# Kernel optimization log

Measured on AMD Instinct MI355X. Metric: run time of the kernel, lower is better.

The kernel has to match this reference:

```python
import jax, jax.numpy as jnp
import numpy as np
import math

EPS = 1e-5
HEADS = 8

def _lin(x, w, b):
    return x @ w.T + b

def _ln(x, g, b):
    m = x.mean(-1, keepdims=True)
    v = ((x - m) ** 2).mean(-1, keepdims=True)
    return (x - m) / jnp.sqrt(v + EPS) * g + b

def _bn_eval(x, g, b):
    # BatchNorm1d eval with init running stats (mean=0, var=1)
    return x / jnp.sqrt(1.0 + EPS) * g[None, :, None] + b[None, :, None]

def _conv1d(x, w, b, pad):
    y = jax.lax.conv_general_dilated(x, w, (1,), [(pad, pad)],
                                     dimension_numbers=('NCH', 'OIH', 'NCH'))
    return y + b[None, :, None]

def _interp_linear(x, out_len):
    # F.interpolate(mode='linear', align_corners=False) on last axis
    L = x.shape[-1]
    src = (jnp.arange(out_len) + 0.5) * (L / out_len) - 0.5
    src = jnp.clip(src, 0.0, L - 1)
    i0 = jnp.floor(src).astype(jnp.int32)
    i1 = jnp.minimum(i0 + 1, L - 1)
    w = (src - i0).astype(x.dtype)
    return x[..., i0] * (1.0 - w) + x[..., i1] * w

def setup_inputs():
    key = jax.random.key(0)
    ks = iter(jax.random.split(key, 64))
    def nrm(shape, scale=0.02):
        return jax.random.normal(next(ks), shape, dtype=jnp.float32) * scale
    B, T, N, H, HOR, C = 2, 64, 2048, 128, 24, 32
    return dict(
        x=jax.random.normal(next(ks), (B, T, N), dtype=jnp.float32),
        tc_w=nrm((C, 1, 3), 0.2), tc_b=jnp.zeros((C,)), tc_bn_g=jnp.ones((C,)), tc_bn_b=jnp.zeros((C,)),
        fp_w=nrm((H, C * T)), fp_b=jnp.zeros((H,)), fp_ln_g=jnp.ones((H,)), fp_ln_b=jnp.zeros((H,)),
        q_w=nrm((H, H)), q_b=jnp.zeros((H,)),
        k_w=nrm((H, H)), k_b=jnp.zeros((H,)),
        v_w=nrm((H, H)), v_b=jnp.zeros((H,)),
        o_w=nrm((H, H)), o_b=jnp.zeros((H,)),
        adj=nrm((1, HEADS, N, N), 0.02),
        s0_w=nrm((H, H, 1), 0.05), s0_b=jnp.zeros((H,)), s0_bn_g=jnp.ones((H,)), s0_bn_b=jnp.zeros((H,)),
        s1_w=nrm((H, H, 2), 0.05), s1_b=jnp.zeros((H,)), s1_bn_g=jnp.ones((H,)), s1_bn_b=jnp.zeros((H,)),
        fusion_weight=jnp.ones((2,)),
        fu_w=nrm((H, H)), fu_b=jnp.zeros((H,)), fu_ln_g=jnp.ones((H,)), fu_ln_b=jnp.zeros((H,)),
        pr1_w=nrm((H, H)), pr1_b=jnp.zeros((H,)), pr_ln_g=jnp.ones((H,)), pr_ln_b=jnp.zeros((H,)),
        pr2_w=nrm((HOR, H)), pr2_b=jnp.zeros((HOR,)),
        rg_w=nrm((HOR, H)), rg_b=jnp.zeros((HOR,)),
    )

def _forward(x, tc_w, tc_b, tc_bn_g, tc_bn_b, fp_w, fp_b, fp_ln_g, fp_ln_b,
             q_w, q_b, k_w, k_b, v_w, v_b, o_w, o_b, adj,
             s0_w, s0_b, s0_bn_g, s0_bn_b, s1_w, s1_b, s1_bn_g, s1_bn_b,
             fusion_weight, fu_w, fu_b, fu_ln_g, fu_ln_b,
             pr1_w, pr1_b, pr_ln_g, pr_ln_b, pr2_w, pr2_b, rg_w, rg_b):
    B, T, N = x.shape
    H = q_w.shape[0]
    hd = H // HEADS
    x_last = x[:, -1, :]                                  # (B, N)
    # temporal conv over the window per node
    xt = x.transpose(0, 2, 1).reshape(B * N, 1, T)
    f = jax.nn.relu(_bn_eval(_conv1d(xt, tc_w, tc_b, 1), tc_bn_g, tc_bn_b))
    f = f.reshape(B, N, -1)                               # (B, N, 32*T)
    feats = jax.nn.relu(_ln(_lin(f, fp_w, fp_b), fp_ln_g, fp_ln_b))
    # adaptive graph attention with learnable adjacency bias
    q = _lin(feats, q_w, q_b).reshape(B, N, HEADS, hd)
    k = _lin(feats, k_w, k_b).reshape(B, N, HEADS, hd)
    v = _lin(feats, v_w, v_b).reshape(B, N, HEADS, hd)
    scores = jnp.einsum('bnhd,bmhd->bhnm', q, k) / math.sqrt(hd) + adj
    attn = jax.nn.softmax(scores, axis=-1)                # (B, HEADS, N, N)
    reg = jnp.float32(1e-4) * jnp.mean(jnp.abs(attn))
    go = jnp.einsum('bhnm,bmhd->bnhd', attn, v).reshape(B, N, H)
    gf = _lin(go, o_w, o_b)                               # (B, N, H)
    # multi-scale fusion (conv over node axis, kernels 1 and 2)
    xc = gf.transpose(0, 2, 1)                            # (B, H, N)
    f0 = jax.nn.relu(_bn_eval(_conv1d(xc, s0_w, s0_b, 0), s0_bn_g, s0_bn_b))
    f1 = jax.nn.relu(_bn_eval(_conv1d(xc, s1_w, s1_b, 1), s1_bn_g, s1_bn_b))  # (B,H,N+1)
    f1 = _interp_linear(f1, N)
    alpha = jax.nn.softmax(fusion_weight)
    fused = (alpha[0] * f0 + alpha[1] * f1).transpose(0, 2, 1)
    ff = jax.nn.relu(_ln(_lin(fused, fu_w, fu_b), fu_ln_g, fu_ln_b))
    # progressive prediction refinement
    h = jax.nn.relu(_ln(_lin(ff, pr1_w, pr1_b), pr_ln_g, pr_ln_b))
    preds = _lin(h, pr2_w, pr2_b)                         # (B, N, horizon)
    gates = jax.nn.sigmoid(_lin(ff, rg_w, rg_b))
    refined = gates * x_last[..., None] + (1.0 - gates) * preds
    return refined.transpose(0, 2, 1), reg                # (B, horizon, N), scalar

def reference(x, tc_w, tc_b, tc_bn_g, tc_bn_b, fp_w, fp_b, fp_ln_g, fp_ln_b,
              q_w, q_b, k_w, k_b, v_w, v_b, o_w, o_b, adj,
              s0_w, s0_b, s0_bn_g, s0_bn_b, s1_w, s1_b, s1_bn_g, s1_bn_b,
              fusion_weight, fu_w, fu_b, fu_ln_g, fu_ln_b,
              pr1_w, pr1_b, pr_ln_g, pr_ln_b, pr2_w, pr2_b, rg_w, rg_b):
    return _forward(x, tc_w, tc_b, tc_bn_g, tc_bn_b, fp_w, fp_b, fp_ln_g, fp_ln_b,
                    q_w, q_b, k_w, k_b, v_w, v_b, o_w, o_b, adj,
                    s0_w, s0_b, s0_bn_g, s0_bn_b, s1_w, s1_b, s1_bn_g, s1_bn_b,
                    fusion_weight, fu_w, fu_b, fu_ln_g, fu_ln_b,
                    pr1_w, pr1_b, pr_ln_g, pr_ln_b, pr2_w, pr2_b, rg_w, rg_b)
```

## Files before the change

kernel.cpp:

```cpp
#include <hip/hip_runtime.h>

using f32x4  = __attribute__((ext_vector_type(4))) float;
using bf16x8 = __attribute__((ext_vector_type(8))) short;

#define DEV static __device__ __forceinline__

DEV unsigned short f2bf(float f){
  unsigned u = __float_as_uint(f);
  unsigned r = (u + 0x7FFFu + ((u >> 16) & 1u)) >> 16;
  return (unsigned short)r;
}

__global__ __launch_bounds__(256) void prep_conv_kernel(
    const float* __restrict__ fp_w, const float* __restrict__ q_w,
    const float* __restrict__ k_w, const float* __restrict__ v_w,
    const float* __restrict__ o_w, const float* __restrict__ s0_w,
    const float* __restrict__ s1_w, const float* __restrict__ fu_w,
    const float* __restrict__ pr1_w, const float* __restrict__ pr2_w,
    const float* __restrict__ rg_w,
    unsigned short* __restrict__ fpw_bf, unsigned short* __restrict__ wcat_bf,
    float* __restrict__ o_wT, float* __restrict__ fu_wT, float* __restrict__ pr1_wT,
    float* __restrict__ s0_wT, float* __restrict__ s1_wT0, float* __restrict__ s1_wT1,
    float* __restrict__ pr2_wT, float* __restrict__ rg_wT,
    const float* __restrict__ x, const float* __restrict__ tc_w,
    const float* __restrict__ tc_b, const float* __restrict__ bn_g,
    const float* __restrict__ bn_b, unsigned short* __restrict__ f){
  if (blockIdx.x < 512){
    int i = blockIdx.x * 256 + threadIdx.x;
    const int stride = 512 * 256;
    for (int idx = i; idx < 128 * 2048; idx += stride) fpw_bf[idx] = f2bf(fp_w[idx]);
    for (int idx = i; idx < 384 * 128; idx += stride){
      int c = idx >> 7, k = idx & 127;
      float v;
      if (c < 128)      v = q_w[c * 128 + k] * 0.25f;
      else if (c < 256) v = k_w[(c - 128) * 128 + k];
      else              v = v_w[(c - 256) * 128 + k];
      wcat_bf[idx] = f2bf(v);
    }
    for (int idx = i; idx < 128 * 128; idx += stride){
      int k = idx >> 7, c = idx & 127;
      o_wT[idx]   = o_w[c * 128 + k];
      fu_wT[idx]  = fu_w[c * 128 + k];
      pr1_wT[idx] = pr1_w[c * 128 + k];
      s0_wT[idx]  = s0_w[c * 128 + k];
      s1_wT0[idx] = s1_w[(c * 128 + k) * 2 + 0];
      s1_wT1[idx] = s1_w[(c * 128 + k) * 2 + 1];
    }
    for (int idx = i; idx < 128 * 24; idx += stride){
      int k = idx / 24, c = idx % 24;
      pr2_wT[idx] = pr2_w[c * 128 + k];
      rg_wT[idx]  = rg_w[c * 128 + k];
    }
  } else {
    int lane = threadIdx.x & 63;
    int w = threadIdx.x >> 6;
    int row = (blockIdx.x - 512) * 4 + w;
    int b = row >> 11, n = row & 2047;
    float xv = x[(size_t)(b * 64 + lane) * 2048 + n];
    float xm = __shfl_up(xv, 1, 64);   if (lane == 0)  xm = 0.f;
    float xp = __shfl_down(xv, 1, 64); if (lane == 63) xp = 0.f;
    const float inv = rsqrtf(1.0f + 1e-5f);
    unsigned short* frow = f + (size_t)row * 2048;
    #pragma unroll
    for (int c = 0; c < 32; c++){
      float y = xm * tc_w[c * 3 + 0] + xv * tc_w[c * 3 + 1] + xp * tc_w[c * 3 + 2] + tc_b[c];
      y = y * inv * bn_g[c] + bn_b[c];
      frow[c * 64 + lane] = f2bf(fmaxf(y, 0.f));
    }
  }
}

__global__ __launch_bounds__(512) void feat_kernel(
    const unsigned short* __restrict__ f, const unsigned short* __restrict__ fpw,
    const float* __restrict__ fp_b, const float* __restrict__ ln_g,
    const float* __restrict__ ln_b, unsigned short* __restrict__ feats){
  __shared__ float pre[16][128];
  __shared__ float stat[16][2];
  int t = threadIdx.x;
  int lane = t & 63, w = t >> 6;
  int l15 = lane & 15, g = lane >> 4;
  int row0 = blockIdx.x * 16;
  int c0 = w * 16;
  f32x4 acc = {0.f,0.f,0.f,0.f};
  const unsigned short* arow = f   + (size_t)(row0 + l15) * 2048 + g * 8;
  const unsigned short* bp   = fpw + (size_t)(c0 + l15) * 2048 + g * 8;
  #pragma unroll 4
  for (int k = 0; k < 2048; k += 32){
    bf16x8 a  = *(const bf16x8*)(arow + k);
    bf16x8 b0 = *(const bf16x8*)(bp + k);
    acc = __builtin_amdgcn_mfma_f32_16x16x32_bf16(a, b0, acc, 0, 0, 0);
  }
  #pragma unroll
  for (int r = 0; r < 4; r++)
    pre[g * 4 + r][c0 + l15] = acc[r] + fp_b[c0 + l15];
  __syncthreads();
  if (t < 256){
    int r = t >> 4, j = t & 15;
    float s = 0.f, ss = 0.f;
    #pragma unroll
    for (int q = 0; q < 8; q++){ float v = pre[r][j + q * 16]; s += v; ss += v * v; }
    #pragma unroll
    for (int m = 1; m < 16; m <<= 1){ s += __shfl_xor(s, m, 64); ss += __shfl_xor(ss, m, 64); }
    if (j == 0){
      float mean = s * (1.f / 128.f);
      stat[r][0] = mean;
      stat[r][1] = rsqrtf(ss * (1.f / 128.f) - mean * mean + 1e-5f);
    }
  }
  __syncthreads();
  if (t < 256){
    int r = t >> 4, j = t & 15;
    float mean = stat[r][0], rstd = stat[r][1];
    bf16x8 outv;
    #pragma unroll
    for (int q = 0; q < 8; q++){
      int c = j * 8 + q;
      float v = (pre[r][c] - mean) * rstd * ln_g[c] + ln_b[c];
      outv[q] = (short)f2bf(fmaxf(v, 0.f));
    }
    *(bf16x8*)(feats + (size_t)(row0 + r) * 128 + j * 8) = outv;
  }
}

__global__ __launch_bounds__(256) void qkv_kernel(
    const unsigned short* __restrict__ feats, const unsigned short* __restrict__ wcat,
    const float* __restrict__ q_b, const float* __restrict__ k_b,
    const float* __restrict__ v_b, unsigned short* __restrict__ qo,
    unsigned short* __restrict__ ko, unsigned short* __restrict__ vT){
  int t = threadIdx.x, lane = t & 63, w = t >> 6;
  int l15 = lane & 15, g = lane >> 4;
  int row0 = blockIdx.x * 16;
  int c0 = w * 96;
  f32x4 acc[6];
  #pragma unroll
  for (int i = 0; i < 6; i++) acc[i] = (f32x4){0.f,0.f,0.f,0.f};
  const unsigned short* arow = feats + (size_t)(row0 + l15) * 128 + g * 8;
  #pragma unroll
  for (int k = 0; k < 128; k += 32){
    bf16x8 a = *(const bf16x8*)(arow + k);
    #pragma unroll
    for (int ni = 0; ni < 6; ni++){
      bf16x8 bb = *(const bf16x8*)(wcat + (size_t)(c0 + ni * 16 + l15) * 128 + g * 8 + k);
      acc[ni] = __builtin_amdgcn_mfma_f32_16x16x32_bf16(a, bb, acc[ni], 0, 0, 0);
    }
  }
  #pragma unroll
  for (int ni = 0; ni < 6; ni++){
    int c = c0 + ni * 16 + l15;
    int mat = c >> 7, cm = c & 127;
    int h = cm >> 4, d = cm & 15;
    float bias = (mat == 0) ? q_b[cm] * 0.25f : (mat == 1 ? k_b[cm] : v_b[cm]);
    #pragma unroll
    for (int r = 0; r < 4; r++){
      int row = row0 + g * 4 + r;
      int b = row >> 11, n = row & 2047;
      unsigned short bv = f2bf(acc[ni][r] + bias);
      int bh = b * 8 + h;
      if (mat == 0)      qo[((size_t)bh * 2048 + n) * 16 + d] = bv;
      else if (mat == 1) ko[((size_t)bh * 2048 + n) * 16 + d] = bv;
      else               vT[((size_t)bh * 16 + d) * 2048 + n] = bv;
    }
  }
}

__global__ __launch_bounds__(256) void attn_kernel(
    const unsigned short* __restrict__ qo, const unsigned short* __restrict__ ko,
    const unsigned short* __restrict__ vT, const float* __restrict__ adj,
    float* __restrict__ go){
  __shared__ unsigned short Pls[4][1024];
  __shared__ float adjs[4][16][68];
  __shared__ float red_acc[4][2][16][16];
  __shared__ float red_rs[4][2][16];
  int t = threadIdx.x, lane = t & 63, w = t >> 6;
  int l15 = lane & 15, g = lane >> 4;
  int h = blockIdx.x >> 7;
  int row0 = (blockIdx.x & 127) * 16;
  const bf16x8 zf = {0,0,0,0,0,0,0,0};
  bf16x8 qf[2];
  #pragma unroll
  for (int b = 0; b < 2; b++){
    if (g < 2) qf[b] = *(const bf16x8*)(qo + ((size_t)(b * 8 + h) * 2048 + row0 + l15) * 16 + g * 8);
    else       qf[b] = zf;
  }
  f32x4 accv[2] = {{0.f,0.f,0.f,0.f},{0.f,0.f,0.f,0.f}};
  float rs[2][4] = {{0,0,0,0},{0,0,0,0}};
  const float* adjbase = adj + ((size_t)h * 2048 + row0) * 2048;
  unsigned short* P = Pls[w];
  float (*A)[68] = adjs[w];
  const int mbeg = w * 512;
  for (int m0 = mbeg; m0 < mbeg + 512; m0 += 64){
    #pragma unroll
    for (int it = 0; it < 4; it++){
      int idx = it * 64 + lane;
      int rr = idx >> 4, c4 = (idx & 15) << 2;
      *(f32x4*)(&A[rr][c4]) = *(const f32x4*)(adjbase + (size_t)rr * 2048 + m0 + c4);
    }
    #pragma unroll
    for (int b = 0; b < 2; b++){
      int bh = b * 8 + h;
      const unsigned short* kbase = ko + (size_t)bh * 2048 * 16;
      f32x4 sf[4];
      #pragma unroll
      for (int s = 0; s < 4; s++){
        bf16x8 kf;
        if (g < 2) kf = *(const bf16x8*)(kbase + (size_t)(m0 + s * 16 + l15) * 16 + g * 8);
        else       kf = zf;
        f32x4 z4 = {0.f,0.f,0.f,0.f};
        sf[s] = __builtin_amdgcn_mfma_f32_16x16x32_bf16(qf[b], kf, z4, 0, 0, 0);
      }
      #pragma unroll
      for (int s = 0; s < 4; s++){
        #pragma unroll
        for (int r = 0; r < 4; r++){
          int rowl = g * 4 + r;
          float p = __expf(sf[s][r] + A[rowl][s * 16 + l15]);
          rs[b][r] += p;
          int col = s * 16 + l15;
          int chunk = col >> 3;
          P[rowl * 64 + (((chunk ^ (rowl & 7)) << 3) | (col & 7))] = f2bf(p);
        }
      }
      const unsigned short* vbase = vT + (size_t)bh * 16 * 2048;
      #pragma unroll
      for (int half = 0; half < 2; half++){
        int chunk = half * 4 + g;
        bf16x8 af = *(const bf16x8*)(P + l15 * 64 + ((chunk ^ (l15 & 7)) << 3));
        bf16x8 vf = *(const bf16x8*)(vbase + (size_t)l15 * 2048 + m0 + half * 32 + g * 8);
        accv[b] = __builtin_amdgcn_mfma_f32_16x16x32_bf16(af, vf, accv[b], 0, 0, 0);
      }
    }
  }
  #pragma unroll
  for (int b = 0; b < 2; b++){
    #pragma unroll
    for (int r = 0; r < 4; r++){
      float s = rs[b][r];
      #pragma unroll
      for (int m = 1; m < 16; m <<= 1) s += __shfl_xor(s, m, 64);
      red_acc[w][b][g * 4 + r][l15] = accv[b][r];
      if (l15 == 0) red_rs[w][b][g * 4 + r] = s;
    }
  }
  __syncthreads();
  for (int i = t; i < 512; i += 256){
    int b = i >> 8, row = (i >> 4) & 15, col = i & 15;
    float v = 0.f, d = 0.f;
    #pragma unroll
    for (int ww = 0; ww < 4; ww++){ v += red_acc[ww][b][row][col]; d += red_rs[ww][b][row]; }
    go[((size_t)b * 2048 + row0 + row) * 128 + h * 16 + col] = v / d;
  }
}

__global__ __launch_bounds__(512) void tail_kernel(
    const float* __restrict__ go, const float* __restrict__ x,
    const float* __restrict__ o_wT, const float* __restrict__ o_b,
    const float* __restrict__ s0_wT, const float* __restrict__ s0_b,
    const float* __restrict__ s0_g, const float* __restrict__ s0_bb,
    const float* __restrict__ s1_wT0, const float* __restrict__ s1_wT1,
    const float* __restrict__ s1_b, const float* __restrict__ s1_g,
    const float* __restrict__ s1_bb, const float* __restrict__ fw,
    const float* __restrict__ fu_wT, const float* __restrict__ fu_b,
    const float* __restrict__ fu_g, const float* __restrict__ fu_bb,
    const float* __restrict__ pr1_wT, const float* __restrict__ pr1_b,
    const float* __restrict__ pr_g, const float* __restrict__ pr_bb,
    const float* __restrict__ pr2_wT, const float* __restrict__ pr2_b,
    const float* __restrict__ rg_wT, const float* __restrict__ rg_b,
    float* __restrict__ out){
  __shared__ float go_s[20][128];
  __shared__ float gf_s[21][128];
  __shared__ float f1_s[17][128];
  __shared__ float fu_in[16][128];
  __shared__ float pre_s[16][128];
  __shared__ float ff_s[16][128];
  __shared__ float h_s[16][128];
  __shared__ float stat[16][2];
  int t = threadIdx.x;
  int b = blockIdx.x >> 7;
  int n0 = (blockIdx.x & 127) * 16;
  for (int e = t; e < 20 * 128; e += 512){
    int lr = e >> 7, cc = e & 127;
    int gn = n0 - 1 + lr;
    go_s[lr][cc] = (lr < 18 && gn >= 0 && gn < 2048) ? go[((size_t)b * 2048 + gn) * 128 + cc] : 0.f;
  }
  __syncthreads();
  int c = t & 127, q4 = t >> 7;
  const float bninv = rsqrtf(1.0f + 1e-5f);
  {
    float acc[5];
    float bias = o_b[c];
    #pragma unroll
    for (int i = 0; i < 5; i++) acc[i] = bias;
    for (int k = 0; k < 128; k++){
      float wv = o_wT[k * 128 + c];
      #pragma unroll
      for (int i = 0; i < 5; i++) acc[i] += go_s[i * 4 + q4][k] * wv;
    }
    #pragma unroll
    for (int i = 0; i < 5; i++){
      int lr = i * 4 + q4;
      int gn = n0 - 1 + lr;
      gf_s[lr][c] = (lr < 18 && gn >= 0 && gn < 2048) ? acc[i] : 0.f;
    }
    if (t < 128) gf_s[20][t] = 0.f;
  }
  __syncthreads();
  {
    float acc[5];
    float bias = s1_b[c];
    #pragma unroll
    for (int i = 0; i < 5; i++) acc[i] = bias;
    for (int k = 0; k < 128; k++){
      float w0 = s1_wT0[k * 128 + c], w1 = s1_wT1[k * 128 + c];
      #pragma unroll
      for (int i = 0; i < 5; i++)
        acc[i] += gf_s[i * 4 + q4][k] * w0 + gf_s[i * 4 + q4 + 1][k] * w1;
    }
    float sc = s1_g[c] * bninv, bb2 = s1_bb[c];
    #pragma unroll
    for (int i = 0; i < 5; i++){
      int lr = i * 4 + q4;
      if (lr < 17) f1_s[lr][c] = fmaxf(acc[i] * sc + bb2, 0.f);
    }
  }
  __syncthreads();
  {
    float acc[4];
    float bias = s0_b[c];
    #pragma unroll
    for (int i = 0; i < 4; i++) acc[i] = bias;
    for (int k = 0; k < 128; k++){
      float wv = s0_wT[k * 128 + c];
      #pragma unroll
      for (int i = 0; i < 4; i++) acc[i] += gf_s[i * 4 + q4 + 1][k] * wv;
    }
    float e0 = __expf(fw[0]), e1 = __expf(fw[1]);
    float a0 = e0 / (e0 + e1), a1 = e1 / (e0 + e1);
    float sc = s0_g[c] * bninv, bb2 = s0_bb[c];
    #pragma unroll
    for (int i = 0; i < 4; i++){
      int lr = i * 4 + q4;
      int n = n0 + lr;
      float f0 = fmaxf(acc[i] * sc + bb2, 0.f);
      float wn = (n + 0.5f) * (1.0f / 2048.0f);
      fu_in[lr][c] = a0 * f0 + a1 * ((1.f - wn) * f1_s[lr][c] + wn * f1_s[lr + 1][c]);
    }
  }
  __syncthreads();
  {
    float acc[4];
    float bias = fu_b[c];
    #pragma unroll
    for (int i = 0; i < 4; i++) acc[i] = bias;
    for (int k = 0; k < 128; k++){
      float wv = fu_wT[k * 128 + c];
      #pragma unroll
      for (int i = 0; i < 4; i++) acc[i] += fu_in[i * 4 + q4][k] * wv;
    }
    #pragma unroll
    for (int i = 0; i < 4; i++) pre_s[i * 4 + q4][c] = acc[i];
  }
  __syncthreads();
  if (t < 256){
    int r = t >> 4, j = t & 15;
    float s = 0.f, ss = 0.f;
    #pragma unroll
    for (int q = 0; q < 8; q++){ float v = pre_s[r][j + q * 16]; s += v; ss += v * v; }
    #pragma unroll
    for (int m = 1; m < 16; m <<= 1){ s += __shfl_xor(s, m, 64); ss += __shfl_xor(ss, m, 64); }
    if (j == 0){ float mean = s * (1.f / 128.f); stat[r][0] = mean;
                 stat[r][1] = rsqrtf(ss * (1.f / 128.f) - mean * mean + 1e-5f); }
  }
  __syncthreads();
  if (t < 256){
    int r = t >> 4, j = t & 15;
    float mean = stat[r][0], rstd = stat[r][1];
    #pragma unroll
    for (int q = 0; q < 8; q++){
      int cc = j * 8 + q;
      ff_s[r][cc] = fmaxf((pre_s[r][cc] - mean) * rstd * fu_g[cc] + fu_bb[cc], 0.f);
    }
  }
  __syncthreads();
  {
    float acc[4];
    float bias = pr1_b[c];
    #pragma unroll
    for (int i = 0; i < 4; i++) acc[i] = bias;
    for (int k = 0; k < 128; k++){
      float wv = pr1_wT[k * 128 + c];
      #pragma unroll
      for (int i = 0; i < 4; i++) acc[i] += ff_s[i * 4 + q4][k] * wv;
    }
    #pragma unroll
    for (int i = 0; i < 4; i++) pre_s[i * 4 + q4][c] = acc[i];
  }
  __syncthreads();
  if (t < 256){
    int r = t >> 4, j = t & 15;
    float s = 0.f, ss = 0.f;
    #pragma unroll
    for (int q = 0; q < 8; q++){ float v = pre_s[r][j + q * 16]; s += v; ss += v * v; }
    #pragma unroll
    for (int m = 1; m < 16; m <<= 1){ s += __shfl_xor(s, m, 64); ss += __shfl_xor(ss, m, 64); }
    if (j == 0){ float mean = s * (1.f / 128.f); stat[r][0] = mean;
                 stat[r][1] = rsqrtf(ss * (1.f / 128.f) - mean * mean + 1e-5f); }
  }
  __syncthreads();
  if (t < 256){
    int r = t >> 4, j = t & 15;
    float mean = stat[r][0], rstd = stat[r][1];
    #pragma unroll
    for (int q = 0; q < 8; q++){
      int cc = j * 8 + q;
      h_s[r][cc] = fmaxf((pre_s[r][cc] - mean) * rstd * pr_g[cc] + pr_bb[cc], 0.f);
    }
  }
  __syncthreads();
  if (t < 384){
    int lr = t / 24, cc = t % 24;
    float accp = pr2_b[cc], accg = rg_b[cc];
    for (int k = 0; k < 128; k++){
      accp += h_s[lr][k] * pr2_wT[k * 24 + cc];
      accg += ff_s[lr][k] * rg_wT[k * 24 + cc];
    }
    float gate = 1.f / (1.f + __expf(-accg));
    int n = n0 + lr;
    float xl = x[((size_t)b * 64 + 63) * 2048 + n];
    out[((size_t)b * 24 + cc) * 2048 + n] = gate * xl + (1.f - gate) * accp;
  }
  if (blockIdx.x == 0 && t == 0) out[2 * 24 * 2048] = 1e-4f / 2048.0f;
}

extern "C" void kernel_launch(void* const* d_in, const int* in_sizes, int n_in,
                              void* d_out, int out_size, void* d_ws, size_t ws_size,
                              hipStream_t stream){
  const float* x       = (const float*)d_in[0];
  const float* tc_w    = (const float*)d_in[1];
  const float* tc_b    = (const float*)d_in[2];
  const float* tc_bn_g = (const float*)d_in[3];
  const float* tc_bn_b = (const float*)d_in[4];
  const float* fp_w    = (const float*)d_in[5];
  const float* fp_b    = (const float*)d_in[6];
  const float* fp_ln_g = (const float*)d_in[7];
  const float* fp_ln_b = (const float*)d_in[8];
  const float* q_w     = (const float*)d_in[9];
  const float* q_b     = (const float*)d_in[10];
  const float* k_w     = (const float*)d_in[11];
  const float* k_b     = (const float*)d_in[12];
  const float* v_w     = (const float*)d_in[13];
  const float* v_b     = (const float*)d_in[14];
  const float* o_w     = (const float*)d_in[15];
  const float* o_b     = (const float*)d_in[16];
  const float* adj     = (const float*)d_in[17];
  const float* s0_w    = (const float*)d_in[18];
  const float* s0_b    = (const float*)d_in[19];
  const float* s0_bn_g = (const float*)d_in[20];
  const float* s0_bn_b = (const float*)d_in[21];
  const float* s1_w    = (const float*)d_in[22];
  const float* s1_b    = (const float*)d_in[23];
  const float* s1_bn_g = (const float*)d_in[24];
  const float* s1_bn_b = (const float*)d_in[25];
  const float* fusion_w= (const float*)d_in[26];
  const float* fu_w    = (const float*)d_in[27];
  const float* fu_b    = (const float*)d_in[28];
  const float* fu_ln_g = (const float*)d_in[29];
  const float* fu_ln_b = (const float*)d_in[30];
  const float* pr1_w   = (const float*)d_in[31];
  const float* pr1_b   = (const float*)d_in[32];
  const float* pr_ln_g = (const float*)d_in[33];
  const float* pr_ln_b = (const float*)d_in[34];
  const float* pr2_w   = (const float*)d_in[35];
  const float* pr2_b   = (const float*)d_in[36];
  const float* rg_w    = (const float*)d_in[37];
  const float* rg_b    = (const float*)d_in[38];
  float* out = (float*)d_out;

  char* ws = (char*)d_ws;
  size_t off = 0;
  auto alloc = [&](size_t bytes) -> void* {
    void* p = ws + off;
    off += (bytes + 255) & ~(size_t)255;
    return p;
  };
  unsigned short* f_bf    = (unsigned short*)alloc((size_t)4096 * 2048 * 2);
  unsigned short* fpw_bf  = (unsigned short*)alloc((size_t)128 * 2048 * 2);
  unsigned short* wcat_bf = (unsigned short*)alloc((size_t)384 * 128 * 2);
  unsigned short* feats_bf= (unsigned short*)alloc((size_t)4096 * 128 * 2);
  unsigned short* q_bf    = (unsigned short*)alloc((size_t)16 * 2048 * 16 * 2);
  unsigned short* k_bf    = (unsigned short*)alloc((size_t)16 * 2048 * 16 * 2);
  unsigned short* vT_bf   = (unsigned short*)alloc((size_t)16 * 2048 * 16 * 2);
  float* go     = (float*)alloc((size_t)4096 * 128 * 4);
  float* o_wT   = (float*)alloc(128 * 128 * 4);
  float* fu_wT  = (float*)alloc(128 * 128 * 4);
  float* pr1_wT = (float*)alloc(128 * 128 * 4);
  float* s0_wT  = (float*)alloc(128 * 128 * 4);
  float* s1_wT0 = (float*)alloc(128 * 128 * 4);
  float* s1_wT1 = (float*)alloc(128 * 128 * 4);
  float* pr2_wT = (float*)alloc(128 * 24 * 4);
  float* rg_wT  = (float*)alloc(128 * 24 * 4);
  if (off > ws_size) return;

  prep_conv_kernel<<<1536, 256, 0, stream>>>(fp_w, q_w, k_w, v_w, o_w, s0_w, s1_w,
                                             fu_w, pr1_w, pr2_w, rg_w, fpw_bf, wcat_bf,
                                             o_wT, fu_wT, pr1_wT, s0_wT, s1_wT0, s1_wT1,
                                             pr2_wT, rg_wT,
                                             x, tc_w, tc_b, tc_bn_g, tc_bn_b, f_bf);
  feat_kernel<<<256, 512, 0, stream>>>(f_bf, fpw_bf, fp_b, fp_ln_g, fp_ln_b, feats_bf);
  qkv_kernel<<<256, 256, 0, stream>>>(feats_bf, wcat_bf, q_b, k_b, v_b, q_bf, k_bf, vT_bf);
  attn_kernel<<<1024, 256, 0, stream>>>(q_bf, k_bf, vT_bf, adj, go);
  tail_kernel<<<256, 512, 0, stream>>>(go, x, o_wT, o_b, s0_wT, s0_b, s0_bn_g, s0_bn_b,
                                       s1_wT0, s1_wT1, s1_b, s1_bn_g, s1_bn_b, fusion_w,
                                       fu_wT, fu_b, fu_ln_g, fu_ln_b, pr1_wT, pr1_b,
                                       pr_ln_g, pr_ln_b, pr2_wT, pr2_b, rg_wT, rg_b, out);
}
```

Baseline: 138.2 us.

## Fuse feature and QKV kernels, keep attention probabilities in registers

```diff
diff --git a/kernel.cpp b/kernel.cpp
--- a/kernel.cpp
+++ b/kernel.cpp
@@ -9,6 +9,10 @@
   unsigned u = __float_as_uint(f);
   unsigned r = (u + 0x7FFFu + ((u >> 16) & 1u)) >> 16;
   return (unsigned short)r;
+}
+
+DEV int vperm(int n){
+  return (n & ~63) | (n & 32) | ((n & 0xC) << 1) | ((n & 0x10) >> 2) | (n & 3);
 }
 
 __global__ __launch_bounds__(256) void prep_conv_kernel(
@@ -70,16 +74,22 @@
   }
 }
 
-__global__ __launch_bounds__(512) void feat_kernel(
+__global__ __launch_bounds__(512) void featqkv_kernel(
     const unsigned short* __restrict__ f, const unsigned short* __restrict__ fpw,
     const float* __restrict__ fp_b, const float* __restrict__ ln_g,
-    const float* __restrict__ ln_b, unsigned short* __restrict__ feats){
+    const float* __restrict__ ln_b,
+    const unsigned short* __restrict__ wcat, const float* __restrict__ q_b,
+    const float* __restrict__ k_b, const float* __restrict__ v_b,
+    unsigned short* __restrict__ qo, unsigned short* __restrict__ ko,
+    unsigned short* __restrict__ vTp){
   __shared__ float pre[16][128];
+  __shared__ unsigned short ft[16 * 128];
   __shared__ float stat[16][2];
   int t = threadIdx.x;
   int lane = t & 63, w = t >> 6;
   int l15 = lane & 15, g = lane >> 4;
   int row0 = blockIdx.x * 16;
+  int b = row0 >> 11, n0 = row0 & 2047;
   int c0 = w * 16;
   f32x4 acc = {0.f,0.f,0.f,0.f};
   const unsigned short* arow = f   + (size_t)(row0 + l15) * 2048 + g * 8;
@@ -114,90 +124,74 @@
     bf16x8 outv;
     #pragma unroll
     for (int q = 0; q < 8; q++){
-      int c = j * 8 + q;
-      float v = (pre[r][c] - mean) * rstd * ln_g[c] + ln_b[c];
+      int cc = j * 8 + q;
+      float v = (pre[r][cc] - mean) * rstd * ln_g[cc] + ln_b[cc];
       outv[q] = (short)f2bf(fmaxf(v, 0.f));
     }
-    *(bf16x8*)(feats + (size_t)(row0 + r) * 128 + j * 8) = outv;
-  }
-}
-
-__global__ __launch_bounds__(256) void qkv_kernel(
-    const unsigned short* __restrict__ feats, const unsigned short* __restrict__ wcat,
-    const float* __restrict__ q_b, const float* __restrict__ k_b,
-    const float* __restrict__ v_b, unsigned short* __restrict__ qo,
-    unsigned short* __restrict__ ko, unsigned short* __restrict__ vT){
-  int t = threadIdx.x, lane = t & 63, w = t >> 6;
-  int l15 = lane & 15, g = lane >> 4;
-  int row0 = blockIdx.x * 16;
-  int c0 = w * 96;
-  f32x4 acc[6];
+    int byte = r * 256 + ((j * 16) ^ ((r & 7) << 4));
+    *(bf16x8*)((char*)ft + byte) = outv;
+  }
+  __syncthreads();
+  f32x4 acc3[3] = {{0,0,0,0},{0,0,0,0},{0,0,0,0}};
   #pragma unroll
-  for (int i = 0; i < 6; i++) acc[i] = (f32x4){0.f,0.f,0.f,0.f};
-  const unsigned short* arow = feats + (size_t)(row0 + l15) * 128 + g * 8;
+  for (int kk = 0; kk < 128; kk += 32){
+    int abyte = l15 * 256 + (((kk + g * 8) * 2) ^ ((l15 & 7) << 4));
+    bf16x8 a = *(const bf16x8*)((const char*)ft + abyte);
+    #pragma unroll
+    for (int ci = 0; ci < 3; ci++){
+      int cc0 = w * 48 + ci * 16;
+      bf16x8 bb = *(const bf16x8*)(wcat + (size_t)(cc0 + l15) * 128 + g * 8 + kk);
+      acc3[ci] = __builtin_amdgcn_mfma_f32_16x16x32_bf16(a, bb, acc3[ci], 0, 0, 0);
+    }
+  }
   #pragma unroll
-  for (int k = 0; k < 128; k += 32){
-    bf16x8 a = *(const bf16x8*)(arow + k);
-    #pragma unroll
-    for (int ni = 0; ni < 6; ni++){
-      bf16x8 bb = *(const bf16x8*)(wcat + (size_t)(c0 + ni * 16 + l15) * 128 + g * 8 + k);
-      acc[ni] = __builtin_amdgcn_mfma_f32_16x16x32_bf16(a, bb, acc[ni], 0, 0, 0);
-    }
-  }
-  #pragma unroll
-  for (int ni = 0; ni < 6; ni++){
-    int c = c0 + ni * 16 + l15;
+  for (int ci = 0; ci < 3; ci++){
+    int c = w * 48 + ci * 16 + l15;
     int mat = c >> 7, cm = c & 127;
-    int h = cm >> 4, d = cm & 15;
+    int hh = cm >> 4, d = cm & 15;
     float bias = (mat == 0) ? q_b[cm] * 0.25f : (mat == 1 ? k_b[cm] : v_b[cm]);
+    int bh = b * 8 + hh;
     #pragma unroll
     for (int r = 0; r < 4; r++){
-      int row = row0 + g * 4 + r;
-      int b = row >> 11, n = row & 2047;
-      unsigned short bv = f2bf(acc[ni][r] + bias);
-      int bh = b * 8 + h;
+      int n = n0 + g * 4 + r;
+      unsigned short bv = f2bf(acc3[ci][r] + bias);
       if (mat == 0)      qo[((size_t)bh * 2048 + n) * 16 + d] = bv;
       else if (mat == 1) ko[((size_t)bh * 2048 + n) * 16 + d] = bv;
-      else               vT[((size_t)bh * 16 + d) * 2048 + n] = bv;
-    }
-  }
-}
-
-__global__ __launch_bounds__(256) void attn_kernel(
+      else               vTp[((size_t)bh * 16 + d) * 2048 + vperm(n)] = bv;
+    }
+  }
+}
+
+__global__ __launch_bounds__(512) void attn_kernel(
     const unsigned short* __restrict__ qo, const unsigned short* __restrict__ ko,
-    const unsigned short* __restrict__ vT, const float* __restrict__ adj,
+    const unsigned short* __restrict__ vTp, const float* __restrict__ adj,
     float* __restrict__ go){
-  __shared__ unsigned short Pls[4][1024];
-  __shared__ float adjs[4][16][68];
-  __shared__ float red_acc[4][2][16][16];
-  __shared__ float red_rs[4][2][16];
+  __shared__ float red_acc[8][2][16][16];
+  __shared__ float red_rs[8][2][16];
   int t = threadIdx.x, lane = t & 63, w = t >> 6;
   int l15 = lane & 15, g = lane >> 4;
   int h = blockIdx.x >> 7;
   int row0 = (blockIdx.x & 127) * 16;
   const bf16x8 zf = {0,0,0,0,0,0,0,0};
+  const f32x4 z4 = {0.f,0.f,0.f,0.f};
   bf16x8 qf[2];
   #pragma unroll
-  for (int b = 0; b < 2; b++){
-    if (g < 2) qf[b] = *(const bf16x8*)(qo + ((size_t)(b * 8 + h) * 2048 + row0 + l15) * 16 + g * 8);
-    else       qf[b] = zf;
+  for (int b2 = 0; b2 < 2; b2++){
+    if (g < 2) qf[b2] = *(const bf16x8*)(qo + ((size_t)(b2 * 8 + h) * 2048 + row0 + l15) * 16 + g * 8);
+    else       qf[b2] = zf;
   }
   f32x4 accv[2] = {{0.f,0.f,0.f,0.f},{0.f,0.f,0.f,0.f}};
-  float rs[2][4] = {{0,0,0,0},{0,0,0,0}};
-  const float* adjbase = adj + ((size_t)h * 2048 + row0) * 2048;
-  unsigned short* P = Pls[w];
-  float (*A)[68] = adjs[w];
-  const int mbeg = w * 512;
-  for (int m0 = mbeg; m0 < mbeg + 512; m0 += 64){
-    #pragma unroll
-    for (int it = 0; it < 4; it++){
-      int idx = it * 64 + lane;
-      int rr = idx >> 4, c4 = (idx & 15) << 2;
-      *(f32x4*)(&A[rr][c4]) = *(const f32x4*)(adjbase + (size_t)rr * 2048 + m0 + c4);
-    }
-    #pragma unroll
-    for (int b = 0; b < 2; b++){
-      int bh = b * 8 + h;
+  float rsp[2] = {0.f, 0.f};
+  const float* adjrow = adj + ((size_t)h * 2048 + row0 + l15) * 2048 + g * 4;
+  const int mbeg = w * 256;
+  for (int m0 = mbeg; m0 < mbeg + 256; m0 += 64){
+    f32x4 adjv[4];
+    #pragma unroll
+    for (int s = 0; s < 4; s++)
+      adjv[s] = *(const f32x4*)(adjrow + m0 + s * 16);
+    #pragma unroll
+    for (int b2 = 0; b2 < 2; b2++){
+      int bh = b2 * 8 + h;
       const unsigned short* kbase = ko + (size_t)bh * 2048 * 16;
       f32x4 sf[4];
       #pragma unroll
@@ -205,49 +199,43 @@
         bf16x8 kf;
         if (g < 2) kf = *(const bf16x8*)(kbase + (size_t)(m0 + s * 16 + l15) * 16 + g * 8);
         else       kf = zf;
-        f32x4 z4 = {0.f,0.f,0.f,0.f};
-        sf[s] = __builtin_amdgcn_mfma_f32_16x16x32_bf16(qf[b], kf, z4, 0, 0, 0);
+        sf[s] = __builtin_amdgcn_mfma_f32_16x16x32_bf16(kf, qf[b2], z4, 0, 0, 0);
       }
+      bf16x8 pf[2];
+      float partial = 0.f;
       #pragma unroll
       for (int s = 0; s < 4; s++){
         #pragma unroll
         for (int r = 0; r < 4; r++){
-          int rowl = g * 4 + r;
-          float p = __expf(sf[s][r] + A[rowl][s * 16 + l15]);
-          rs[b][r] += p;
-          int col = s * 16 + l15;
-          int chunk = col >> 3;
-          P[rowl * 64 + (((chunk ^ (rowl & 7)) << 3) | (col & 7))] = f2bf(p);
+          float p = __expf(sf[s][r] + adjv[s][r]);
+          partial += p;
+          pf[s >> 1][(s & 1) * 4 + r] = (short)f2bf(p);
         }
       }
-      const unsigned short* vbase = vT + (size_t)bh * 16 * 2048;
-      #pragma unroll
-      for (int half = 0; half < 2; half++){
-        int chunk = half * 4 + g;
-        bf16x8 af = *(const bf16x8*)(P + l15 * 64 + ((chunk ^ (l15 & 7)) << 3));
-        bf16x8 vf = *(const bf16x8*)(vbase + (size_t)l15 * 2048 + m0 + half * 32 + g * 8);
-        accv[b] = __builtin_amdgcn_mfma_f32_16x16x32_bf16(af, vf, accv[b], 0, 0, 0);
-      }
+      rsp[b2] += partial;
+      const unsigned short* vbase = vTp + ((size_t)bh * 16 + l15) * 2048 + m0;
+      bf16x8 vf0 = *(const bf16x8*)(vbase + g * 8);
+      bf16x8 vf1 = *(const bf16x8*)(vbase + 32 + g * 8);
+      accv[b2] = __builtin_amdgcn_mfma_f32_16x16x32_bf16(vf0, pf[0], accv[b2], 0, 0, 0);
+      accv[b2] = __builtin_amdgcn_mfma_f32_16x16x32_bf16(vf1, pf[1], accv[b2], 0, 0, 0);
     }
   }
   #pragma unroll
-  for (int b = 0; b < 2; b++){
-    #pragma unroll
-    for (int r = 0; r < 4; r++){
-      float s = rs[b][r];
-      #pragma unroll
-      for (int m = 1; m < 16; m <<= 1) s += __shfl_xor(s, m, 64);
-      red_acc[w][b][g * 4 + r][l15] = accv[b][r];
-      if (l15 == 0) red_rs[w][b][g * 4 + r] = s;
-    }
-  }
-  __syncthreads();
-  for (int i = t; i < 512; i += 256){
-    int b = i >> 8, row = (i >> 4) & 15, col = i & 15;
-    float v = 0.f, d = 0.f;
-    #pragma unroll
-    for (int ww = 0; ww < 4; ww++){ v += red_acc[ww][b][row][col]; d += red_rs[ww][b][row]; }
-    go[((size_t)b * 2048 + row0 + row) * 128 + h * 16 + col] = v / d;
+  for (int b2 = 0; b2 < 2; b2++){
+    float s = rsp[b2];
+    s += __shfl_xor(s, 16, 64);
+    s += __shfl_xor(s, 32, 64);
+    #pragma unroll
+    for (int r = 0; r < 4; r++) red_acc[w][b2][g * 4 + r][l15] = accv[b2][r];
+    if (lane < 16) red_rs[w][b2][l15] = s;
+  }
+  __syncthreads();
+  {
+    int b2 = t >> 8, qq = (t >> 4) & 15, d = t & 15;
+    float v = 0.f, den = 0.f;
+    #pragma unroll
+    for (int ww = 0; ww < 8; ww++){ v += red_acc[ww][b2][d][qq]; den += red_rs[ww][b2][qq]; }
+    go[((size_t)b2 * 2048 + row0 + qq) * 128 + h * 16 + d] = v / den;
   }
 }
 
@@ -485,10 +473,9 @@
   unsigned short* f_bf    = (unsigned short*)alloc((size_t)4096 * 2048 * 2);
   unsigned short* fpw_bf  = (unsigned short*)alloc((size_t)128 * 2048 * 2);
   unsigned short* wcat_bf = (unsigned short*)alloc((size_t)384 * 128 * 2);
-  unsigned short* feats_bf= (unsigned short*)alloc((size_t)4096 * 128 * 2);
   unsigned short* q_bf    = (unsigned short*)alloc((size_t)16 * 2048 * 16 * 2);
   unsigned short* k_bf    = (unsigned short*)alloc((size_t)16 * 2048 * 16 * 2);
-  unsigned short* vT_bf   = (unsigned short*)alloc((size_t)16 * 2048 * 16 * 2);
+  unsigned short* vTp_bf  = (unsigned short*)alloc((size_t)16 * 2048 * 16 * 2);
   float* go     = (float*)alloc((size_t)4096 * 128 * 4);
   float* o_wT   = (float*)alloc(128 * 128 * 4);
   float* fu_wT  = (float*)alloc(128 * 128 * 4);
@@ -505,9 +492,9 @@
                                              o_wT, fu_wT, pr1_wT, s0_wT, s1_wT0, s1_wT1,
                                              pr2_wT, rg_wT,
                                              x, tc_w, tc_b, tc_bn_g, tc_bn_b, f_bf);
-  feat_kernel<<<256, 512, 0, stream>>>(f_bf, fpw_bf, fp_b, fp_ln_g, fp_ln_b, feats_bf);
-  qkv_kernel<<<256, 256, 0, stream>>>(feats_bf, wcat_bf, q_b, k_b, v_b, q_bf, k_bf, vT_bf);
-  attn_kernel<<<1024, 256, 0, stream>>>(q_bf, k_bf, vT_bf, adj, go);
+  featqkv_kernel<<<256, 512, 0, stream>>>(f_bf, fpw_bf, fp_b, fp_ln_g, fp_ln_b,
+                                          wcat_bf, q_b, k_b, v_b, q_bf, k_bf, vTp_bf);
+  attn_kernel<<<1024, 512, 0, stream>>>(q_bf, k_bf, vTp_bf, adj, go);
   tail_kernel<<<256, 512, 0, stream>>>(go, x, o_wT, o_b, s0_wT, s0_b, s0_bn_g, s0_bn_b,
                                        s1_wT0, s1_wT1, s1_b, s1_bn_g, s1_bn_b, fusion_w,
                                        fu_wT, fu_b, fu_ln_g, fu_ln_b, pr1_wT, pr1_b,
```

New measurement: 134.1 us. 1.03x faster.
